# Optimization experiments

Measured on AMD Instinct MI355X. Metric: run time of the kernel, lower is better.

Reference implementation:

```python
import jax, jax.numpy as jnp
import numpy as np

D = 256      # input_dim
C = 10       # n_classes
T = 15       # n_trees
DEPTH = 4    # tree_depth
H = 5        # n_heads
I = 2 ** DEPTH - 1   # internal nodes = 15
L = 2 ** DEPTH       # leaves = 16
ENC = 64
P = T * I * (D + 1) + T * L * C + T  # 60240
NS, NQ = 2048, 32768


def _ln(x, g, b):
    # torch LayerNorm: biased variance, eps=1e-5
    m = x.mean(-1, keepdims=True)
    v = x.var(-1, keepdims=True)
    return (x - m) * jax.lax.rsqrt(v + 1e-5) * g + b


def setup_inputs() -> dict:
    key = jax.random.key(0)
    ks = jax.random.split(key, 8)
    s = 0.05
    return {
        "X_support": jax.random.normal(ks[0], (NS, D), jnp.float32),
        "X_query": jax.random.normal(ks[1], (NQ, D), jnp.float32),
        "enc_w1": jax.random.normal(ks[2], (H, D, ENC), jnp.float32) * s,
        "enc_b1": jnp.zeros((H, ENC), jnp.float32),
        "ln1_g": jnp.ones((H, ENC), jnp.float32),
        "ln1_b": jnp.zeros((H, ENC), jnp.float32),
        "enc_w2": jax.random.normal(ks[3], (H, ENC, ENC), jnp.float32) * s,
        "enc_b2": jnp.zeros((H, ENC), jnp.float32),
        "ln2_g": jnp.ones((H, ENC), jnp.float32),
        "ln2_b": jnp.zeros((H, ENC), jnp.float32),
        "pg_w1": jax.random.normal(ks[4], (H, ENC, 128), jnp.float32) * s,
        "pg_b1": jnp.zeros((H, 128), jnp.float32),
        "pg_ln_g": jnp.ones((H, 128), jnp.float32),
        "pg_ln_b": jnp.zeros((H, 128), jnp.float32),
        "pg_w2": jax.random.normal(ks[5], (H, 128, P), jnp.float32) * s,
        "pg_b2": jnp.zeros((H, P), jnp.float32),
        "head_weights": jnp.ones((H,), jnp.float32) / H,
        "temperature": jnp.ones((1,), jnp.float32),
    }


def reference(X_support, X_query, enc_w1, enc_b1, ln1_g, ln1_b, enc_w2, enc_b2,
              ln2_g, ln2_b, pg_w1, pg_b1, pg_ln_g, pg_ln_b, pg_w2, pg_b2,
              head_weights, temperature):
    gelu = lambda x: jax.nn.gelu(x, approximate=False)  # torch default GELU (erf)
    head_w = jax.nn.softmax(head_weights)  # [H]

    # ---- data encoders (all heads batched; dropout=eval/no-op) ----
    h = jnp.einsum('nd,hde->hne', X_support, enc_w1) + enc_b1[:, None, :]
    h = gelu(_ln(h, ln1_g[:, None, :], ln1_b[:, None, :]))
    h = jnp.einsum('hne,hef->hnf', h, enc_w2) + enc_b2[:, None, :]
    h = gelu(_ln(h, ln2_g[:, None, :], ln2_b[:, None, :]))
    ctx = h.mean(axis=1)  # [H, ENC] (context = support mean)

    # ---- param generators ----
    p = jnp.einsum('he,hef->hf', ctx, pg_w1) + pg_b1
    p = gelu(_ln(p, pg_ln_g, pg_ln_b))
    params = jnp.tanh(jnp.einsum('hf,hfp->hp', p, pg_w2) + pg_b2) * 2.0  # [H, P]

    sw, sb, lf = T * I * D, T * I, T * L * C
    split_w = params[:, :sw].reshape(H, T, I, D)
    split_b = params[:, sw:sw + sb].reshape(H, T, I)
    leaf_logits = params[:, sw + sb:sw + sb + lf].reshape(H, T, L, C)
    tree_w = jax.nn.softmax(params[:, sw + sb + lf:], axis=-1)  # [H, T]

    temp = jnp.clip(temperature[0], 0.1, 2.0)

    # ---- all split decisions in one batched matmul: [H, T, Nq, I] ----
    dec = jax.nn.sigmoid(
        (jnp.einsum('nd,htid->htni', X_query, split_w) + split_b[:, :, None, :]) / temp)

    # ---- parallel branching-probability sweep over depth ----
    N = X_query.shape[0]
    reach = jnp.ones((H, T, N, 1), dtype=X_query.dtype)
    for d in range(DEPTH):  # static, small loop
        start, n = 2 ** d - 1, 2 ** d
        dsl = dec[..., start:start + n]                        # [H,T,N,n]
        # interleave (parent*(1-dec), parent*dec) exactly like torch cat order
        reach = jnp.stack([reach * (1.0 - dsl), reach * dsl], axis=-1).reshape(H, T, N, 2 * n)

    leaf_p = jax.nn.softmax(leaf_logits / temp, axis=-1)        # [H,T,L,C]
    pred = jnp.einsum('htnl,htlc->htnc', reach, leaf_p)         # [H,T,N,C]
    out = jnp.einsum('htnc,ht,h->nc', pred, tree_w, head_w)     # [N,C]
    return out
```

## Files before the change

### kernel.cpp

```cpp
#include <hip/hip_runtime.h>

#define DEV __device__ __forceinline__

typedef __attribute__((ext_vector_type(8))) short short8;
typedef __attribute__((ext_vector_type(4))) float f32x4;
typedef __attribute__((ext_vector_type(4))) unsigned short ushort4_t;
typedef __attribute__((ext_vector_type(4))) unsigned int uint4_t;

namespace {
constexpr int D_ = 256, C_ = 10, T_ = 15, H_ = 5, ENC_ = 64, L_ = 16;
constexpr int NS_ = 2048, NQ_ = 32768;
constexpr int P_ = 60240, SW_ = 57600, SB_ = 225, LF_ = 2400;
constexpr int FEAT_ = 128;
constexpr int G_ = 75;
constexpr int GSPLIT_ = 2;
constexpr int WGB_ = 16384;
constexpr int NBLK_ = 128;

constexpr size_t OFF_CP   = 0;
constexpr size_t OFF_PVEC = OFF_CP + (size_t)H_*NBLK_*ENC_;
constexpr size_t OFF_TMP  = OFF_PVEC + (size_t)H_*FEAT_;
constexpr size_t OFF_SB   = OFF_TMP + 8;
constexpr size_t OFF_LRAW = OFF_SB + (size_t)G_*16 + 16;
constexpr size_t OFF_TRAW = OFF_LRAW + (size_t)H_*T_*L_*C_;
constexpr size_t OFF_SL   = OFF_TRAW + (size_t)H_*T_;
constexpr size_t OFF_WBF  = OFF_SL + (size_t)H_*T_*L_*C_;
constexpr size_t OFF_SLA  = OFF_WBF + (size_t)G_*WGB_/4;
constexpr size_t OFF_OUTP = OFF_SLA + (size_t)G_*1024/4;
constexpr size_t WS_NEED_FLOATS = OFF_OUTP + (size_t)GSPLIT_*NQ_*10;
}

DEV float wave_sum(float v) {
  #pragma unroll
  for (int o = 32; o; o >>= 1) v += __shfl_xor(v, o, 64);
  return v;
}
DEV float gelu_exact(float x) { return 0.5f * x * (1.f + erff(x * 0.70710678118654752f)); }
DEV unsigned short f2bf(float x) {
  unsigned u = __float_as_uint(x);
  return (unsigned short)((u + 0x7FFFu + ((u >> 16) & 1u)) >> 16);
}
DEV float bf2f(unsigned short b) { return __uint_as_float(((unsigned)b) << 16); }
DEV unsigned cvt_pk_bf16(float lo, float hi) {
  unsigned d;
  asm("v_cvt_pk_bf16_f32 %0, %1, %2" : "=v"(d) : "v"(lo), "v"(hi));
  return d;
}
DEV float fast_rcp(float x) {
  float r;
  asm("v_rcp_f32 %0, %1" : "=v"(r) : "v"(x));
  return r;
}
DEV void gload16(const char* g, char* l) {
  __builtin_amdgcn_global_load_lds(
      (const __attribute__((address_space(1))) void*)g,
      (__attribute__((address_space(3))) void*)l, 16, 0, 0);
}

__global__ __launch_bounds__(256) void enc12_kernel(
    const float* __restrict__ Xbase,
    const float* __restrict__ W1, const float* __restrict__ B1,
    const float* __restrict__ G1, const float* __restrict__ Be1,
    const float* __restrict__ W2, const float* __restrict__ B2,
    const float* __restrict__ G2, const float* __restrict__ Be2,
    float* __restrict__ Partial)
{
  __shared__ float xs[4][4][ENC_];
  __shared__ float red[4][ENC_];
  const int h = blockIdx.y;
  const int lane = threadIdx.x & 63;
  const int wv = threadIdx.x >> 6;
  const int row0 = blockIdx.x * 16 + wv * 4;

  {
    constexpr int K = 256;
    const float* __restrict__ X = Xbase + (size_t)row0 * K;
    const float* __restrict__ wc = W1 + (size_t)h * K * ENC_ + lane;
    float a0 = 0.f, a1 = 0.f, a2 = 0.f, a3 = 0.f;
    #pragma unroll 4
    for (int k = 0; k < K; ++k) {
      const float wkl = wc[(size_t)k * ENC_];
      a0 = fmaf(X[k],       wkl, a0);
      a1 = fmaf(X[K + k],   wkl, a1);
      a2 = fmaf(X[2*K + k], wkl, a2);
      a3 = fmaf(X[3*K + k], wkl, a3);
    }
    const float bb = B1[h*ENC_ + lane];
    const float gg = G1[h*ENC_ + lane], be = Be1[h*ENC_ + lane];
    float acc[4] = {a0 + bb, a1 + bb, a2 + bb, a3 + bb};
    #pragma unroll
    for (int r = 0; r < 4; ++r) {
      const float m = wave_sum(acc[r]) * (1.f / ENC_);
      const float d = acc[r] - m;
      const float var = wave_sum(d * d) * (1.f / ENC_);
      const float y = d * rsqrtf(var + 1e-5f) * gg + be;
      xs[wv][r][lane] = gelu_exact(y);
    }
  }
  __syncthreads();
  {
    constexpr int K = 64;
    const float* __restrict__ wc = W2 + (size_t)h * K * ENC_ + lane;
    float a0 = 0.f, a1 = 0.f, a2 = 0.f, a3 = 0.f;
    #pragma unroll 4
    for (int k = 0; k < K; ++k) {
      const float wkl = wc[(size_t)k * ENC_];
      a0 = fmaf(xs[wv][0][k], wkl, a0);
      a1 = fmaf(xs[wv][1][k], wkl, a1);
      a2 = fmaf(xs[wv][2][k], wkl, a2);
      a3 = fmaf(xs[wv][3][k], wkl, a3);
    }
    const float bb = B2[h*ENC_ + lane];
    const float gg = G2[h*ENC_ + lane], be = Be2[h*ENC_ + lane];
    float acc[4] = {a0 + bb, a1 + bb, a2 + bb, a3 + bb};
    float psum = 0.f;
    #pragma unroll
    for (int r = 0; r < 4; ++r) {
      const float m = wave_sum(acc[r]) * (1.f / ENC_);
      const float d = acc[r] - m;
      const float var = wave_sum(d * d) * (1.f / ENC_);
      const float y = d * rsqrtf(var + 1e-5f) * gg + be;
      psum += gelu_exact(y);
    }
    red[wv][lane] = psum;
    __syncthreads();
    if (wv == 0) {
      const float tot = red[0][lane] + red[1][lane] + red[2][lane] + red[3][lane];
      Partial[((size_t)h * NBLK_ + blockIdx.x) * ENC_ + lane] = tot;
    }
  }
}

__global__ __launch_bounds__(128) void pvec_kernel(
    const float* __restrict__ Partial, const float* __restrict__ temperature,
    const float* __restrict__ w1, const float* __restrict__ b1,
    const float* __restrict__ g, const float* __restrict__ b,
    float* __restrict__ pvec, float* __restrict__ tmp)
{
  __shared__ float red[128];
  __shared__ float ctxl[ENC_];
  __shared__ float sred[2];
  const int h = blockIdx.x, tid = threadIdx.x;
  const int e = tid & 63, half = tid >> 6;
  float s = 0.f;
  const float* __restrict__ pp = Partial + (size_t)h * NBLK_ * ENC_ + e;
  #pragma unroll 4
  for (int bb = half * 64; bb < half * 64 + 64; ++bb) s += pp[(size_t)bb * ENC_];
  red[tid] = s;
  __syncthreads();
  if (half == 0) ctxl[e] = (red[e] + red[64 + e]) * (1.f / NS_);
  if (h == 0 && tid == 0) {
    const float t = fminf(fmaxf(temperature[0], 0.1f), 2.0f);
    tmp[0] = t; tmp[1] = 1.f / t;
  }
  __syncthreads();
  const int j = tid;
  float acc = b1[h * FEAT_ + j];
  #pragma unroll 4
  for (int e2 = 0; e2 < ENC_; ++e2)
    acc = fmaf(ctxl[e2], w1[((size_t)h * ENC_ + e2) * FEAT_ + j], acc);
  const int lane = j & 63, wvv = j >> 6;
  const float ps = wave_sum(acc);
  if (lane == 0) sred[wvv] = ps;
  __syncthreads();
  const float m = (sred[0] + sred[1]) * (1.f / FEAT_);
  const float d = acc - m;
  const float vs = wave_sum(d * d);
  __syncthreads();
  if (lane == 0) sred[wvv] = vs;
  __syncthreads();
  const float var = (sred[0] + sred[1]) * (1.f / FEAT_);
  const float y = d * rsqrtf(var + 1e-5f) * g[h * FEAT_ + j] + b[h * FEAT_ + j];
  pvec[h * FEAT_ + j] = gelu_exact(y);
}

__global__ __launch_bounds__(256) void params_kernel(
    const float* __restrict__ pvec, const float* __restrict__ w2,
    const float* __restrict__ b2, const float* __restrict__ tmp,
    char* __restrict__ WbfB, float* __restrict__ sbv,
    float* __restrict__ lraw, float* __restrict__ traw)
{
  __shared__ float pl[FEAT_];
  const int h = blockIdx.y;
  if (threadIdx.x < FEAT_) pl[threadIdx.x] = pvec[h * FEAT_ + threadIdx.x];
  __syncthreads();
  const int j4 = blockIdx.x * 1024 + threadIdx.x * 4;
  if (j4 >= P_) return;
  const float it = tmp[1];
  float4 acc = *reinterpret_cast<const float4*>(b2 + (size_t)h * P_ + j4);
  const float* __restrict__ wp = w2 + (size_t)h * FEAT_ * P_ + j4;
  #pragma unroll 4
  for (int k = 0; k < FEAT_; ++k) {
    const float pk = pl[k];
    const float4 wv = *reinterpret_cast<const float4*>(wp + (size_t)k * P_);
    acc.x = fmaf(pk, wv.x, acc.x);
    acc.y = fmaf(pk, wv.y, acc.y);
    acc.z = fmaf(pk, wv.z, acc.z);
    acc.w = fmaf(pk, wv.w, acc.w);
  }
  const float vals[4] = {acc.x, acc.y, acc.z, acc.w};
  if (j4 < SW_) {
    const int t = j4 / 3840, rem = j4 - t * 3840, i = rem >> 8, d = rem & 255;
    const int g = h * T_ + t;
    ushort4_t hs, ls;
    #pragma unroll
    for (int q = 0; q < 4; ++q) {
      const float v = tanhf(vals[q]) * 2.f * it;
      const unsigned short hb = f2bf(v);
      hs[q] = hb;
      ls[q] = f2bf(v - bf2f(hb));
    }
    const unsigned off = (unsigned)(i * 512 + d * 2) ^ ((unsigned)(i & 15) << 4);
    char* base = WbfB + (size_t)g * WGB_;
    *(ushort4_t*)(base + off) = hs;
    *(ushort4_t*)(base + 8192 + off) = ls;
  } else {
    #pragma unroll
    for (int q = 0; q < 4; ++q) {
      const int j = j4 + q;
      const float v = tanhf(vals[q]) * 2.f;
      if (j < SW_ + SB_) {
        const int jj = j - SW_;
        sbv[((size_t)h * T_ + jj / 15) * 16 + (jj % 15)] = v * it;
      }
      else if (j < SW_ + SB_ + LF_) lraw[h * LF_ + (j - SW_ - SB_)] = v;
      else                          traw[h * T_ + (j - SW_ - SB_ - LF_)] = v;
    }
  }
}

__global__ __launch_bounds__(256) void finalize_kernel(
    const float* __restrict__ head_weights, const float* __restrict__ traw,
    const float* __restrict__ lraw, const float* __restrict__ tmp,
    float* __restrict__ sl, char* __restrict__ slA, char* __restrict__ WbfB,
    float* __restrict__ sbv)
{
  const int g = blockIdx.x;
  const int h = g / T_;
  const int tid = threadIdx.x;
  __shared__ float wtg;
  if (tid < 128) {
    char* base = WbfB + (size_t)g * WGB_ + 15 * 512 + tid * 4;
    *(unsigned*)base = 0u;
    *(unsigned*)(base + 8192) = 0u;
  } else if (tid == 128) {
    sbv[g * 16 + 15] = 0.f;
  } else if (tid == 129) {
    float m = -1e30f;
    for (int hh = 0; hh < H_; ++hh) m = fmaxf(m, head_weights[hh]);
    float s = 0.f;
    for (int hh = 0; hh < H_; ++hh) s += __expf(head_weights[hh] - m);
    const float hwv = __expf(head_weights[h] - m) / s;
    float mt = -1e30f;
    for (int t = 0; t < T_; ++t) mt = fmaxf(mt, traw[h * T_ + t]);
    float st = 0.f;
    for (int t = 0; t < T_; ++t) st += __expf(traw[h * T_ + t] - mt);
    wtg = hwv * __expf(traw[g] - mt) / st;
  }
  __syncthreads();
  const float it = tmp[1];
  if (tid < L_) {
    const int row = g * L_ + tid;
    const float* __restrict__ lr = lraw + (size_t)row * C_;
    float m = -1e30f;
    #pragma unroll
    for (int c = 0; c < C_; ++c) m = fmaxf(m, lr[c]);
    float e[C_]; float s = 0.f;
    #pragma unroll
    for (int c = 0; c < C_; ++c) { e[c] = __expf((lr[c] - m) * it); s += e[c]; }
    const float sc = wtg / s;
    #pragma unroll
    for (int c = 0; c < C_; ++c) sl[(size_t)row * C_ + c] = e[c] * sc;
  }
  __syncthreads();
  if (tid < 64) {
    const int p = tid, c = p & 15, kg = p >> 4;
    ushort4_t w0, w1;
    #pragma unroll
    for (int j = 0; j < 8; ++j) {
      const int l = kg * 8 + j;
      const unsigned short v = (l < 16 && c < 10) ? f2bf(sl[(size_t)(g * 16 + l) * C_ + c]) : (unsigned short)0;
      if (j < 4) w0[j] = v; else w1[j - 4] = v;
    }
    *(ushort4_t*)(slA + (size_t)(g * 64 + p) * 16) = w0;
    *(ushort4_t*)(slA + (size_t)(g * 64 + p) * 16 + 8) = w1;
  }
}

__global__ __launch_bounds__(256, 2) void qk_kernel(
    const float* __restrict__ Xq, const char* __restrict__ WbfB,
    const char* __restrict__ slA, const float* __restrict__ sbvP,
    float* __restrict__ outP)
{
  __shared__ char lds[40960];
  const int tid  = threadIdx.x;
  const int lane = tid & 63;
  const int wv   = tid >> 6;
  const int n0   = blockIdx.x * 128;
  const int gc   = blockIdx.y;
  const int gbeg = gc ? 38 : 0;
  const int gend = gc ? G_ : 38;
  const int lrow = lane & 15;
  const int lkg  = lane >> 4;

  short8 Ah[2][8], Al[2][8];
  #pragma unroll
  for (int rt = 0; rt < 2; ++rt) {
    const float* xr = Xq + (size_t)(n0 + wv * 32 + rt * 16 + lrow) * 256 + lkg * 8;
    #pragma unroll
    for (int ks = 0; ks < 8; ++ks) {
      const f32x4 a = *(const f32x4*)(xr + ks * 32);
      const f32x4 b = *(const f32x4*)(xr + ks * 32 + 4);
      short8 hh, ll;
      #pragma unroll
      for (int j = 0; j < 4; ++j) {
        unsigned short hb = f2bf(a[j]);
        hh[j] = (short)hb; ll[j] = (short)f2bf(a[j] - bf2f(hb));
        hb = f2bf(b[j]);
        hh[4 + j] = (short)hb; ll[4 + j] = (short)f2bf(b[j] - bf2f(hb));
      }
      Ah[rt][ks] = hh; Al[rt][ks] = ll;
    }
  }

  auto DMA = [&](int g, int buf) {
    const char* src = WbfB + (size_t)g * WGB_;
    char* dst = lds + buf * WGB_;
    #pragma unroll
    for (int it = 0; it < 4; ++it) {
      const int seg = wv * 4096 + it * 1024;
      gload16(src + seg + lane * 16, dst + seg);
    }
  };

  DMA(gbeg, 0);
  __syncthreads();

  char* tw = lds + 32768 + wv * 2048;
  const int q  = lane & 15;
  const int h2 = lkg >> 1;

  const int sI1 = 1 + h2, sI2 = 3 + lkg, sI3 = 7 + 2 * lkg, sI4 = 8 + 2 * lkg;
  auto twAddr = [&](int c, int qt) -> unsigned {
    return (unsigned)(c * 128 + qt * 4) ^ ((unsigned)(c & 7) << 4);
  };
  const unsigned tA0_0 = twAddr(0, q),        tA0_1 = twAddr(0, 16 + q);
  const unsigned tA1_0 = twAddr(sI1, q),      tA1_1 = twAddr(sI1, 16 + q);
  const unsigned tA2_0 = twAddr(sI2, q),      tA2_1 = twAddr(sI2, 16 + q);
  const unsigned tA3_0 = twAddr(sI3, q),      tA3_1 = twAddr(sI3, 16 + q);
  const unsigned tA4_0 = twAddr(sI4, q),      tA4_1 = twAddr(sI4, 16 + q);
  const int idx0 = ((lkg & 1) << 5) + q;
  const int idx1 = idx0 + 16;
  const bool act = (lkg < 2);
  const unsigned wA0 = (unsigned)(lrow * 128 + (0 * 16 + lkg * 4) * 4) ^ ((unsigned)(lrow & 7) << 4);
  const unsigned wA1 = (unsigned)(lrow * 128 + (1 * 16 + lkg * 4) * 4) ^ ((unsigned)(lrow & 7) << 4);

  f32x4 Cac0 = {0.f, 0.f, 0.f, 0.f}, Cac1 = {0.f, 0.f, 0.f, 0.f};

  int cur = 0;
  for (int g = gbeg; g < gend; ++g) {
    const short8 Asl = *(const short8*)(slA + (size_t)g * 1024 + lane * 16);
    const float* sbg = sbvP + (size_t)g * 16;
    const float s0v = sbg[0], s1v = sbg[sI1], s2v = sbg[sI2], s3v = sbg[sI3], s4v = sbg[sI4];
    if (g + 1 < gend) DMA(g + 1, cur ^ 1);

    const char* bb = lds + cur * WGB_;
    f32x4 Ch0 = {0,0,0,0}, Cm10 = {0,0,0,0}, Cm20 = {0,0,0,0};
    f32x4 Ch1 = {0,0,0,0}, Cm11 = {0,0,0,0}, Cm21 = {0,0,0,0};
    __builtin_amdgcn_s_setprio(1);
    #pragma unroll
    for (int ks = 0; ks < 8; ++ks) {
      const unsigned adr = (unsigned)(lrow * 512 + ks * 64 + lkg * 16) ^ ((unsigned)lrow << 4);
      const short8 bh = *(const short8*)(bb + adr);
      const short8 bl = *(const short8*)(bb + 8192 + adr);
      Ch0  = __builtin_amdgcn_mfma_f32_16x16x32_bf16(Ah[0][ks], bh, Ch0,  0, 0, 0);
      Cm10 = __builtin_amdgcn_mfma_f32_16x16x32_bf16(Ah[0][ks], bl, Cm10, 0, 0, 0);
      Cm20 = __builtin_amdgcn_mfma_f32_16x16x32_bf16(Al[0][ks], bh, Cm20, 0, 0, 0);
      Ch1  = __builtin_amdgcn_mfma_f32_16x16x32_bf16(Ah[1][ks], bh, Ch1,  0, 0, 0);
      Cm11 = __builtin_amdgcn_mfma_f32_16x16x32_bf16(Ah[1][ks], bl, Cm11, 0, 0, 0);
      Cm21 = __builtin_amdgcn_mfma_f32_16x16x32_bf16(Al[1][ks], bh, Cm21, 0, 0, 0);
    }
    __builtin_amdgcn_s_setprio(0);
    {
      f32x4 cs0, cs1;
      #pragma unroll
      for (int r = 0; r < 4; ++r) { cs0[r] = Ch0[r] + Cm10[r] + Cm20[r]; cs1[r] = Ch1[r] + Cm11[r] + Cm21[r]; }
      *(f32x4*)(tw + wA0) = cs0;
      *(f32x4*)(tw + wA1) = cs1;
    }
    auto leaf = [&](unsigned a0, unsigned a1, unsigned a2, unsigned a3, unsigned a4, f32x4& CacT) {
      const float lg0 = *(const float*)(tw + a0) + s0v;
      const float lg1 = *(const float*)(tw + a1) + s1v;
      const float lg2 = *(const float*)(tw + a2) + s2v;
      const float lg3 = *(const float*)(tw + a3) + s3v;
      const float lg4 = *(const float*)(tw + a4) + s4v;
      const float d0 = fast_rcp(1.f + __expf(-lg0));
      const float d1 = fast_rcp(1.f + __expf(-lg1));
      const float d2 = fast_rcp(1.f + __expf(-lg2));
      const float d3 = fast_rcp(1.f + __expf(-lg3));
      const float d4 = fast_rcp(1.f + __expf(-lg4));
      const float aq = (lkg >= 2) ? d0 : (1.f - d0);
      const float bq = aq * ((lkg & 1) ? d1 : (1.f - d1));
      const float c0 = bq * (1.f - d2), c1 = bq * d2;
      const float r0 = c0 * (1.f - d3), r1 = c0 * d3;
      const float r2 = c1 * (1.f - d4), r3 = c1 * d4;
      const unsigned Pa = cvt_pk_bf16(r0, r1);
      const unsigned Pb = cvt_pk_bf16(r2, r3);
      const unsigned g0w = __shfl(Pa, idx0, 64);
      const unsigned g1w = __shfl(Pb, idx0, 64);
      const unsigned g2w = __shfl(Pa, idx1, 64);
      const unsigned g3w = __shfl(Pb, idx1, 64);
      uint4_t bu;
      bu[0] = act ? g0w : 0u;
      bu[1] = act ? g1w : 0u;
      bu[2] = act ? g2w : 0u;
      bu[3] = act ? g3w : 0u;
      const short8 B0 = __builtin_bit_cast(short8, bu);
      CacT = __builtin_amdgcn_mfma_f32_16x16x32_bf16(Asl, B0, CacT, 0, 0, 0);
    };
    leaf(tA0_0, tA1_0, tA2_0, tA3_0, tA4_0, Cac0);
    leaf(tA0_1, tA1_1, tA2_1, tA3_1, tA4_1, Cac1);
    __syncthreads();
    cur ^= 1;
  }

  float* base = outP + (size_t)gc * ((size_t)NQ_ * 10);
  #pragma unroll
  for (int j = 0; j < 4; ++j) {
    const int c = lkg * 4 + j;
    if (c < 10) {
      base[(size_t)(n0 + wv * 32 + q) * 10 + c]      = Cac0[j];
      base[(size_t)(n0 + wv * 32 + 16 + q) * 10 + c] = Cac1[j];
    }
  }
}

__global__ __launch_bounds__(256) void reduce_kernel(const float* __restrict__ p, float* __restrict__ out)
{
  const size_t i = ((size_t)blockIdx.x * 256 + threadIdx.x) * 4;
  const f32x4 a = *(const f32x4*)(p + i);
  const f32x4 b = *(const f32x4*)(p + (size_t)NQ_ * 10 + i);
  f32x4 s;
  #pragma unroll
  for (int j = 0; j < 4; ++j) s[j] = a[j] + b[j];
  *(f32x4*)(out + i) = s;
}

__global__ void mark_kernel(float* out, float v) { out[threadIdx.x] = v; }

extern "C" void kernel_launch(void* const* d_in, const int* in_sizes, int n_in,
                              void* d_out, int out_size, void* d_ws, size_t ws_size,
                              hipStream_t stream) {
  (void)in_sizes; (void)n_in; (void)out_size;
  const float* Xs          = (const float*)d_in[0];
  const float* Xq          = (const float*)d_in[1];
  const float* enc_w1      = (const float*)d_in[2];
  const float* enc_b1      = (const float*)d_in[3];
  const float* ln1_g       = (const float*)d_in[4];
  const float* ln1_b       = (const float*)d_in[5];
  const float* enc_w2      = (const float*)d_in[6];
  const float* enc_b2      = (const float*)d_in[7];
  const float* ln2_g       = (const float*)d_in[8];
  const float* ln2_b       = (const float*)d_in[9];
  const float* pg_w1       = (const float*)d_in[10];
  const float* pg_b1       = (const float*)d_in[11];
  const float* pg_ln_g     = (const float*)d_in[12];
  const float* pg_ln_b     = (const float*)d_in[13];
  const float* pg_w2       = (const float*)d_in[14];
  const float* pg_b2       = (const float*)d_in[15];
  const float* head_wts    = (const float*)d_in[16];
  const float* temperature = (const float*)d_in[17];

  float* ws   = (float*)d_ws;
  float* cpart= ws + OFF_CP;
  float* pvec = ws + OFF_PVEC;
  float* tmp  = ws + OFF_TMP;
  float* sbp  = ws + OFF_SB;
  float* lrw  = ws + OFF_LRAW;
  float* trw  = ws + OFF_TRAW;
  float* slp  = ws + OFF_SL;
  char*  wbf  = (char*)(ws + OFF_WBF);
  char*  slA  = (char*)(ws + OFF_SLA);
  float* outP = ws + OFF_OUTP;
  float* outp = (float*)d_out;

  unsigned mask = 0;
  (void)hipGetLastError();
  if (ws_size < WS_NEED_FLOATS * sizeof(float)) mask |= 0x80u;

  if (!mask) {
    enc12_kernel<<<dim3(NBLK_, 5), 256, 0, stream>>>(Xs, enc_w1, enc_b1, ln1_g, ln1_b,
                                                     enc_w2, enc_b2, ln2_g, ln2_b, cpart);
    if (hipGetLastError() != hipSuccess) mask |= 1u;
    pvec_kernel<<<5, 128, 0, stream>>>(cpart, temperature, pg_w1, pg_b1, pg_ln_g, pg_ln_b, pvec, tmp);
    if (hipGetLastError() != hipSuccess) mask |= 2u;
    params_kernel<<<dim3(59, 5), 256, 0, stream>>>(pvec, pg_w2, pg_b2, tmp, wbf, sbp, lrw, trw);
    if (hipGetLastError() != hipSuccess) mask |= 4u;
    finalize_kernel<<<G_, 256, 0, stream>>>(head_wts, trw, lrw, tmp, slp, slA, wbf, sbp);
    if (hipGetLastError() != hipSuccess) mask |= 8u;
    qk_kernel<<<dim3(NQ_ / 128, GSPLIT_), 256, 0, stream>>>(Xq, wbf, slA, sbp, outP);
    if (hipGetLastError() != hipSuccess) mask |= 16u;
    reduce_kernel<<<(NQ_ * 10) / (256 * 4), 256, 0, stream>>>(outP, outp);
    if (hipGetLastError() != hipSuccess) mask |= 32u;
  }
  if (mask) {
    mark_kernel<<<1, 16, 0, stream>>>(outp, 1024.f + 4.f * (float)mask);
    (void)hipGetLastError();
  }
}
```

Measured before the change: 156.7 us.

## Triple-buffer weight DMA and prefetch per-group leaf/bias operands one iteration ahead

Moves the split-weight LDS staging in the query kernel from double to triple buffering, so each group's tile is requested two iterations ahead. It replaces __syncthreads with a partial vmcnt wait plus a raw s_barrier, so loads still in flight are not drained at every barrier. The leaf-probability A operand and split biases for the next group are also loaded one iteration early into registers. In exchange, LDS per block grows from 40 KB to 56 KB, which may reduce occupancy against the two-blocks-per-CU launch bound, and correctness now depends on the hand-counted vmcnt values.

```diff
diff --git a/kernel.cpp b/kernel.cpp
--- a/kernel.cpp
+++ b/kernel.cpp
@@ -292,7 +292,7 @@
     const char* __restrict__ slA, const float* __restrict__ sbvP,
     float* __restrict__ outP)
 {
-  __shared__ char lds[40960];
+  __shared__ char lds[57344];
   const int tid  = threadIdx.x;
   const int lane = tid & 63;
   const int wv   = tid >> 6;
@@ -333,10 +333,7 @@
     }
   };
 
-  DMA(gbeg, 0);
-  __syncthreads();
-
-  char* tw = lds + 32768 + wv * 2048;
+  char* tw = lds + 49152 + wv * 2048;
   const int q  = lane & 15;
   const int h2 = lkg >> 1;
 
@@ -357,12 +354,29 @@
 
   f32x4 Cac0 = {0.f, 0.f, 0.f, 0.f}, Cac1 = {0.f, 0.f, 0.f, 0.f};
 
+  short8 Acur = *(const short8*)(slA + (size_t)gbeg * 1024 + lane * 16);
+  float s0v, s1v, s2v, s3v, s4v;
+  {
+    const float* sbg = sbvP + (size_t)gbeg * 16;
+    s0v = sbg[0]; s1v = sbg[sI1]; s2v = sbg[sI2]; s3v = sbg[sI3]; s4v = sbg[sI4];
+  }
+  DMA(gbeg, 0);
+  DMA(gbeg + 1, 1);
+  asm volatile("s_waitcnt vmcnt(4)" ::: "memory");
+  __builtin_amdgcn_s_barrier();
+  __builtin_amdgcn_sched_barrier(0);
+
   int cur = 0;
   for (int g = gbeg; g < gend; ++g) {
-    const short8 Asl = *(const short8*)(slA + (size_t)g * 1024 + lane * 16);
-    const float* sbg = sbvP + (size_t)g * 16;
-    const float s0v = sbg[0], s1v = sbg[sI1], s2v = sbg[sI2], s3v = sbg[sI3], s4v = sbg[sI4];
-    if (g + 1 < gend) DMA(g + 1, cur ^ 1);
+    const bool more = (g + 1 < gend);
+    short8 Anx = {};
+    float n0v = 0.f, n1v = 0.f, n2v = 0.f, n3v = 0.f, n4v = 0.f;
+    if (more) {
+      Anx = *(const short8*)(slA + (size_t)(g + 1) * 1024 + lane * 16);
+      const float* sbg = sbvP + (size_t)(g + 1) * 16;
+      n0v = sbg[0]; n1v = sbg[sI1]; n2v = sbg[sI2]; n3v = sbg[sI3]; n4v = sbg[sI4];
+    }
+    if (g + 2 < gend) DMA(g + 2, (cur + 2) % 3);
 
     const char* bb = lds + cur * WGB_;
     f32x4 Ch0 = {0,0,0,0}, Cm10 = {0,0,0,0}, Cm20 = {0,0,0,0};
@@ -416,12 +430,20 @@
       bu[2] = act ? g2w : 0u;
       bu[3] = act ? g3w : 0u;
       const short8 B0 = __builtin_bit_cast(short8, bu);
-      CacT = __builtin_amdgcn_mfma_f32_16x16x32_bf16(Asl, B0, CacT, 0, 0, 0);
+      CacT = __builtin_amdgcn_mfma_f32_16x16x32_bf16(Acur, B0, CacT, 0, 0, 0);
     };
     leaf(tA0_0, tA1_0, tA2_0, tA3_0, tA4_0, Cac0);
     leaf(tA0_1, tA1_1, tA2_1, tA3_1, tA4_1, Cac1);
-    __syncthreads();
-    cur ^= 1;
+
+    if (more) {
+      if (g + 2 < gend) { asm volatile("s_waitcnt vmcnt(4)" ::: "memory"); }
+      else              { asm volatile("s_waitcnt vmcnt(0)" ::: "memory"); }
+      __builtin_amdgcn_s_barrier();
+      __builtin_amdgcn_sched_barrier(0);
+      Acur = Anx;
+      s0v = n0v; s1v = n1v; s2v = n2v; s3v = n3v; s4v = n4v;
+      cur = (cur + 1) % 3;
+    }
   }
 
   float* base = outP + (size_t)gc * ((size_t)NQ_ * 10);
```

Result: slower. 166.9 us (+6.5%).

## Process two weight groups per iteration with quad-buffered LDS prefetch

Applied to the files above, without the earlier changes.

The query kernel's group loop now handles two weight groups per iteration. It uses four 16KB LDS weight buffers and two logit scratch areas, so both groups' MFMA products and both leaf epilogues can be interleaved, and one block barrier covers two groups instead of one. It also prefetches the next pair of groups while the current pair is computed, and a tail path handles an odd leftover group. The aim is to cut barrier count and expose more independent work to hide DMA and epilogue latency. The cost is doubled LDS per block (80KB), which caps occupancy at two blocks per CU, plus higher register pressure.

```diff
diff --git a/kernel.cpp b/kernel.cpp
--- a/kernel.cpp
+++ b/kernel.cpp
@@ -292,7 +292,7 @@
     const char* __restrict__ slA, const float* __restrict__ sbvP,
     float* __restrict__ outP)
 {
-  __shared__ char lds[40960];
+  __shared__ char lds[81920];
   const int tid  = threadIdx.x;
   const int lane = tid & 63;
   const int wv   = tid >> 6;
@@ -333,10 +333,8 @@
     }
   };
 
-  DMA(gbeg, 0);
-  __syncthreads();
-
-  char* tw = lds + 32768 + wv * 2048;
+  char* tw0 = lds + 65536 + wv * 2048;
+  char* tw1 = tw0 + 8192;
   const int q  = lane & 15;
   const int h2 = lkg >> 1;
 
@@ -357,14 +355,7 @@
 
   f32x4 Cac0 = {0.f, 0.f, 0.f, 0.f}, Cac1 = {0.f, 0.f, 0.f, 0.f};
 
-  int cur = 0;
-  for (int g = gbeg; g < gend; ++g) {
-    const short8 Asl = *(const short8*)(slA + (size_t)g * 1024 + lane * 16);
-    const float* sbg = sbvP + (size_t)g * 16;
-    const float s0v = sbg[0], s1v = sbg[sI1], s2v = sbg[sI2], s3v = sbg[sI3], s4v = sbg[sI4];
-    if (g + 1 < gend) DMA(g + 1, cur ^ 1);
-
-    const char* bb = lds + cur * WGB_;
+  auto QKT = [&](const char* bb, char* twp) {
     f32x4 Ch0 = {0,0,0,0}, Cm10 = {0,0,0,0}, Cm20 = {0,0,0,0};
     f32x4 Ch1 = {0,0,0,0}, Cm11 = {0,0,0,0}, Cm21 = {0,0,0,0};
     __builtin_amdgcn_s_setprio(1);
@@ -381,19 +372,20 @@
       Cm21 = __builtin_amdgcn_mfma_f32_16x16x32_bf16(Al[1][ks], bh, Cm21, 0, 0, 0);
     }
     __builtin_amdgcn_s_setprio(0);
-    {
-      f32x4 cs0, cs1;
-      #pragma unroll
-      for (int r = 0; r < 4; ++r) { cs0[r] = Ch0[r] + Cm10[r] + Cm20[r]; cs1[r] = Ch1[r] + Cm11[r] + Cm21[r]; }
-      *(f32x4*)(tw + wA0) = cs0;
-      *(f32x4*)(tw + wA1) = cs1;
-    }
+    f32x4 cs0, cs1;
+    #pragma unroll
+    for (int r = 0; r < 4; ++r) { cs0[r] = Ch0[r] + Cm10[r] + Cm20[r]; cs1[r] = Ch1[r] + Cm11[r] + Cm21[r]; }
+    *(f32x4*)(twp + wA0) = cs0;
+    *(f32x4*)(twp + wA1) = cs1;
+  };
+  auto EPI = [&](const char* twp, short8 AslG,
+                 float s0v, float s1v, float s2v, float s3v, float s4v) {
     auto leaf = [&](unsigned a0, unsigned a1, unsigned a2, unsigned a3, unsigned a4, f32x4& CacT) {
-      const float lg0 = *(const float*)(tw + a0) + s0v;
-      const float lg1 = *(const float*)(tw + a1) + s1v;
-      const float lg2 = *(const float*)(tw + a2) + s2v;
-      const float lg3 = *(const float*)(tw + a3) + s3v;
-      const float lg4 = *(const float*)(tw + a4) + s4v;
+      const float lg0 = *(const float*)(twp + a0) + s0v;
+      const float lg1 = *(const float*)(twp + a1) + s1v;
+      const float lg2 = *(const float*)(twp + a2) + s2v;
+      const float lg3 = *(const float*)(twp + a3) + s3v;
+      const float lg4 = *(const float*)(twp + a4) + s4v;
       const float d0 = fast_rcp(1.f + __expf(-lg0));
       const float d1 = fast_rcp(1.f + __expf(-lg1));
       const float d2 = fast_rcp(1.f + __expf(-lg2));
@@ -416,12 +408,41 @@
       bu[2] = act ? g2w : 0u;
       bu[3] = act ? g3w : 0u;
       const short8 B0 = __builtin_bit_cast(short8, bu);
-      CacT = __builtin_amdgcn_mfma_f32_16x16x32_bf16(Asl, B0, CacT, 0, 0, 0);
+      CacT = __builtin_amdgcn_mfma_f32_16x16x32_bf16(AslG, B0, CacT, 0, 0, 0);
     };
     leaf(tA0_0, tA1_0, tA2_0, tA3_0, tA4_0, Cac0);
     leaf(tA0_1, tA1_1, tA2_1, tA3_1, tA4_1, Cac1);
+  };
+
+  DMA(gbeg, 0);
+  if (gbeg + 1 < gend) DMA(gbeg + 1, 1);
+  __syncthreads();
+
+  int pb = 0;
+  int g = gbeg;
+  for (; g + 1 < gend; g += 2) {
+    const short8 Asl0 = *(const short8*)(slA + (size_t)g * 1024 + lane * 16);
+    const short8 Asl1 = *(const short8*)(slA + (size_t)(g + 1) * 1024 + lane * 16);
+    const float* sb0 = sbvP + (size_t)g * 16;
+    const float* sb1 = sbvP + (size_t)(g + 1) * 16;
+    const float a0v = sb0[0], a1v = sb0[sI1], a2v = sb0[sI2], a3v = sb0[sI3], a4v = sb0[sI4];
+    const float b0v = sb1[0], b1v = sb1[sI1], b2v = sb1[sI2], b3v = sb1[sI3], b4v = sb1[sI4];
+    const int nb = pb ^ 2;
+    if (g + 2 < gend) DMA(g + 2, nb);
+    if (g + 3 < gend) DMA(g + 3, nb + 1);
+    QKT(lds + pb * WGB_, tw0);
+    QKT(lds + (pb + 1) * WGB_, tw1);
+    EPI(tw0, Asl0, a0v, a1v, a2v, a3v, a4v);
+    EPI(tw1, Asl1, b0v, b1v, b2v, b3v, b4v);
     __syncthreads();
-    cur ^= 1;
+    pb ^= 2;
+  }
+  if (g < gend) {
+    const short8 Asl0 = *(const short8*)(slA + (size_t)g * 1024 + lane * 16);
+    const float* sb0 = sbvP + (size_t)g * 16;
+    const float a0v = sb0[0], a1v = sb0[sI1], a2v = sb0[sI2], a3v = sb0[sI3], a4v = sb0[sI4];
+    QKT(lds + pb * WGB_, tw0);
+    EPI(tw0, Asl0, a0v, a1v, a2v, a3v, a4v);
   }
 
   float* base = outP + (size_t)gc * ((size_t)NQ_ * 10);
```

Result: faster. 151.8 us (median of 2 runs) (-3.1%).
